# Kernel optimization log

Measured on AMD Instinct MI355X. Metric: run time of the kernel, lower is better.

The kernel has to match this reference:

```python
import jax, jax.numpy as jnp
import numpy as np

D = 512      # input_dim == encoder d_model
E = 512      # embedding_dim (codebook dim)
V = 8192     # num_embeddings
NC = 1       # num_codebooks
L = 6        # encoder layers
H = 8        # heads
F = 2048     # ffn dim
HD = D // H
EPS = 1e-5


def layernorm(x, s, b):
    m = jnp.mean(x, -1, keepdims=True)
    v = jnp.mean((x - m) ** 2, -1, keepdims=True)
    return (x - m) * jax.lax.rsqrt(v + EPS) * s + b


def sinusoidal_pe(T):
    pos = np.arange(T, dtype=np.float32)[:, None]
    i = np.arange(0, D, 2, dtype=np.float32)[None, :]
    ang = pos / np.power(10000.0, i / D)
    pe = np.zeros((T, D), np.float32)
    pe[:, 0::2] = np.sin(ang)
    pe[:, 1::2] = np.cos(ang)
    return jnp.asarray(pe)


def setup_inputs():
    key = jax.random.key(0)
    ks = jax.random.split(key, 12)
    B, T = 8, 1024
    xs = jax.random.normal(ks[0], (B, T, D), jnp.float32)
    xs_lens = (T // 2 + jax.random.randint(ks[1], (B,), 0, T // 2)).astype(jnp.int32)
    mask_indices = jax.random.uniform(ks[2], (B, T)) < 0.12  # span-mask surrogate
    sc = lambda k, shape, s=0.02: jax.random.normal(k, shape, jnp.float32) * s
    return {
        "xs": xs, "xs_lens": xs_lens, "mask_indices": mask_indices,
        "W_embed": sc(ks[3], (D, D), D ** -0.5),
        "ln1_s": jnp.ones((L, D)), "ln1_b": jnp.zeros((L, D)),
        "Wqkv": sc(ks[4], (L, D, 3 * D)), "Wo": sc(ks[5], (L, D, D)),
        "ln2_s": jnp.ones((L, D)), "ln2_b": jnp.zeros((L, D)),
        "W1": sc(ks[6], (L, D, F)), "W2": sc(ks[7], (L, F, D)),
        "an_s": jnp.ones((D,)), "an_b": jnp.zeros((D,)),
        "iln_s": jnp.ones((D,)), "iln_b": jnp.zeros((D,)),
        "mask_emb": sc(ks[8], (D,), 0.1),
        "top_n_out": sc(ks[9], (NC, D, V)),
        "projection": sc(ks[10], (D, E), (2.0 / (D + E)) ** 0.5),  # xavier_normal, frozen
        "embeddings": jax.random.normal(ks[11], (NC, E, V), jnp.float32),  # frozen codebook
    }


def encoder_blocks(x, pad_mask, ln1_s, ln1_b, Wqkv, Wo, ln2_s, ln2_b, W1, W2, an_s, an_b):
    B, T, _ = x.shape
    attn_bias = jnp.where(pad_mask, 0.0, -1e9)[:, None, None, :]  # [B,1,1,T]

    def layer(x, p):
        l1s, l1b, wqkv, wo, l2s, l2b, w1, w2 = p
        h = layernorm(x, l1s, l1b)
        q, k, v = jnp.split(h @ wqkv, 3, axis=-1)
        q = q.reshape(B, T, H, HD)
        k = k.reshape(B, T, H, HD)
        v = v.reshape(B, T, H, HD)
        scores = jnp.einsum('bqhd,bkhd->bhqk', q, k) * (HD ** -0.5) + attn_bias
        o = jnp.einsum('bhqk,bkhd->bqhd', jax.nn.softmax(scores, axis=-1), v)
        x = x + o.reshape(B, T, D) @ wo
        h = layernorm(x, l2s, l2b)
        x = x + jax.nn.relu(h @ w1) @ w2
        return x, None

    x, _ = jax.lax.scan(layer, x, (ln1_s, ln1_b, Wqkv, Wo, ln2_s, ln2_b, W1, W2))
    return layernorm(x, an_s, an_b)


def nearest_ids(x, iln_s, iln_b, projection, embeddings):
    # layernorm -> projection -> squared-distance argmin per codebook
    B, T, _ = x.shape
    z = layernorm(x, iln_s, iln_b) @ projection        # [B,T,E]
    flat = z.reshape(-1, E)                            # [N,E]
    d = (jnp.sum(flat ** 2, 1)[None, :, None]
         + jnp.sum(embeddings ** 2, 1)[:, None, :]
         - 2.0 * jnp.einsum('ne,gev->gnv', flat, embeddings))  # [NC,N,V]
    return jnp.argmin(d, -1).T.reshape(B, T, NC)


def reference(xs, xs_lens, mask_indices, W_embed, ln1_s, ln1_b, Wqkv, Wo, ln2_s, ln2_b,
              W1, W2, an_s, an_b, iln_s, iln_b, mask_emb, top_n_out, projection, embeddings):
    B, T, _ = xs.shape
    pad_mask = jnp.arange(T)[None, :] < xs_lens[:, None]              # [B,T]
    x = xs @ W_embed + sinusoidal_pe(T)[None]                         # encoder.embed
    target_ids = nearest_ids(x, iln_s, iln_b, projection, embeddings)  # [B,T,NC]
    masked_xs = jnp.where(mask_indices[..., None], mask_emb, x)
    out = encoder_blocks(masked_xs, pad_mask, ln1_s, ln1_b, Wqkv, Wo,
                         ln2_s, ln2_b, W1, W2, an_s, an_b)            # [B,T,D]
    logits = jnp.einsum('btd,gdv->bgtv', out, top_n_out)              # [B,NC,T,V]
    lsm = jax.nn.log_softmax(logits, axis=-1)
    tgt = jnp.transpose(target_ids, (0, 2, 1))                        # [B,NC,T]
    ent = -jnp.take_along_axis(lsm, tgt[..., None], axis=-1)[..., 0]  # [B,NC,T]
    m = (pad_mask & mask_indices).astype(jnp.float32)                 # [B,T]
    loss = jnp.sum(ent * m[:, None, :]) / (jnp.sum(m) * NC)
    return loss
```

## Files before the change

kernel.cpp:

```cpp
#include <hip/hip_runtime.h>
#include <hip/hip_bf16.h>

#define D_ 512
#define T_ 1024
#define B_ 8
#define H_ 8
#define F_ 2048
#define V_ 8192
#define L_ 6
#define NTOK 8192
#define EPS_ 1e-5f
#define NCAP 2048

typedef short short8 __attribute__((ext_vector_type(8)));
typedef float floatx4 __attribute__((ext_vector_type(4)));

__device__ __forceinline__ float bf2f(unsigned short u) {
  union { unsigned int i; float f; } v; v.i = ((unsigned int)u) << 16; return v.f;
}
__device__ __forceinline__ unsigned short f2bf(float f) {
  unsigned int u = __float_as_uint(f);
  return (unsigned short)((u + 0x7fffu + ((u >> 16) & 1u)) >> 16);
}
__device__ __forceinline__ float ldf(const void* p, long long i, int bf) {
  if (bf) return bf2f(((const unsigned short*)p)[i]);
  return ((const float*)p)[i];
}
__device__ __forceinline__ void ld16(const unsigned short* g, unsigned short* l) {
  __builtin_amdgcn_global_load_lds(
      (const __attribute__((address_space(1))) unsigned int*)g,
      (__attribute__((address_space(3))) unsigned int*)l, 16, 0, 0);
}
__device__ __forceinline__ unsigned int fkey(float f) {
  unsigned int u = __float_as_uint(f);
  return (u & 0x80000000u) ? ~u : (u ^ 0x80000000u);
}

__global__ void detect_kernel(const unsigned int* xsw, const unsigned int* mw, int* flags) {
  __shared__ int cnt[256];
  __shared__ int m01[256], mlo[256], mhi[256];
  int tid = threadIdx.x;
  int c = 0;
  for (int t = tid; t < 1024; t += 256) {
    unsigned int lo = xsw[t] & 0xffffu;
    int ok;
    if (lo == 0u) ok = 1;
    else { unsigned int e = (lo >> 7) & 0xffu; ok = (e >= 90u && e <= 140u); }
    c += ok;
  }
  int n01 = 0, lo38 = 0, hi38 = 0;
  for (int t = tid; t < 2048; t += 256) {
    unsigned int w = mw[t];
    if (w > 1u) n01 = 1;
    if ((w & 0xffffu) == 0x3f80u) lo38 = 1;
    if ((w >> 16) == 0x3f80u) hi38 = 1;
  }
  cnt[tid] = c; m01[tid] = n01; mlo[tid] = lo38; mhi[tid] = hi38;
  __syncthreads();
  for (int s = 128; s > 0; s >>= 1) {
    if (tid < s) {
      cnt[tid] += cnt[tid + s];
      m01[tid] |= m01[tid + s]; mlo[tid] |= mlo[tid + s]; mhi[tid] |= mhi[tid + s];
    }
    __syncthreads();
  }
  if (tid == 0) {
    flags[0] = (cnt[0] > 700) ? 1 : 0;
    int fmt;
    if (!m01[0]) fmt = 0;
    else if (mlo[0]) fmt = 2;
    else if (mhi[0]) fmt = 3;
    else fmt = 1;
    flags[1] = fmt;
  }
}

__global__ void conv_all_kernel(const void* d4, const void* d5, const void* d8,
                                const void* d9, const void* d12, const void* d13,
                                const void* d14, const void* d15, const void* d16,
                                float* P, const int* flags) {
  int i = blockIdx.x * 256 + threadIdx.x;
  if (i >= 14848) return;
  int bf = flags[0];
  const void* src; int off;
  if (i < 3072) { src = d4; off = 0; }
  else if (i < 6144) { src = d5; off = 3072; }
  else if (i < 9216) { src = d8; off = 6144; }
  else if (i < 12288) { src = d9; off = 9216; }
  else if (i < 12800) { src = d12; off = 12288; }
  else if (i < 13312) { src = d13; off = 12800; }
  else if (i < 13824) { src = d14; off = 13312; }
  else if (i < 14336) { src = d15; off = 13824; }
  else { src = d16; off = 14336; }
  P[i] = ldf(src, i - off, bf);
}

__global__ void convb_kernel(const void* src, unsigned short* dst, int n, const int* flags) {
  int i = blockIdx.x * 256 + threadIdx.x;
  if (i < n) {
    if (flags[0]) dst[i] = ((const unsigned short*)src)[i];
    else dst[i] = f2bf(((const float*)src)[i]);
  }
}

__global__ __launch_bounds__(256) void trans_kernel(const void* src, unsigned short* dst,
                                                    int K, int N, const int* flags) {
  int bf = flags[0];
  __shared__ unsigned short tile[32][33];
  int n0 = blockIdx.x * 32, k0 = blockIdx.y * 32, batch = blockIdx.z;
  long long sbase = (long long)batch * K * N;
  long long dbase = (long long)batch * N * K;
  int c = threadIdx.x & 31, r8 = threadIdx.x >> 5;
#pragma unroll
  for (int rr = 0; rr < 4; ++rr) {
    int r = r8 + rr * 8;
    tile[r][c] = f2bf(ldf(src, sbase + (long long)(k0 + r) * N + n0 + c, bf));
  }
  __syncthreads();
#pragma unroll
  for (int rr = 0; rr < 4; ++rr) {
    int nn = r8 + rr * 8;
    dst[dbase + (long long)(n0 + nn) * K + k0 + c] = tile[c][nn];
  }
}

__global__ __launch_bounds__(256) void trans_big_kernel(const void* top, const void* emb,
                                                        unsigned short* TOPT, unsigned short* EMBT,
                                                        float* en, const int* flags) {
  int bf = flags[0];
  __shared__ unsigned short tile[32][33];
  int n0 = blockIdx.x * 32, k0 = blockIdx.y * 32, z = blockIdx.z;
  const void* src = z ? emb : top;
  unsigned short* dst = z ? EMBT : TOPT;
  int c = threadIdx.x & 31, r8 = threadIdx.x >> 5;
#pragma unroll
  for (int rr = 0; rr < 4; ++rr) {
    int r = r8 + rr * 8;
    tile[r][c] = f2bf(ldf(src, (long long)(k0 + r) * V_ + n0 + c, bf));
  }
  __syncthreads();
#pragma unroll
  for (int rr = 0; rr < 4; ++rr) {
    int nn = r8 + rr * 8;
    dst[(long long)(n0 + nn) * D_ + k0 + c] = tile[c][nn];
  }
  if (z == 1 && threadIdx.x < 32) {
    int nn = threadIdx.x;
    float s = 0.f;
#pragma unroll
    for (int r = 0; r < 32; ++r) { float x = bf2f(tile[r][nn]); s += x * x; }
    atomicAdd(&en[n0 + nn], s);
  }
}

__global__ void prep_kernel(const void* mask, const int* lens, int* maski, float* mcomb,
                            int* idx, int* cnt, const int* flags) {
  int i = blockIdx.x * 256 + threadIdx.x;
  if (i >= NTOK) return;
  int fmt = flags[1];
  int mi;
  if (fmt == 0) mi = ((const int*)mask)[i] != 0;
  else if (fmt == 1) mi = ((const unsigned char*)mask)[i] != 0;
  else if (fmt == 2) mi = ((const unsigned short*)mask)[i] != 0;
  else mi = ((const float*)mask)[i] != 0.f;
  int b = i >> 10, t = i & (T_ - 1);
  int act = mi && (t < lens[b]);
  maski[i] = mi;
  mcomb[i] = act ? 1.f : 0.f;
  if (act) {
    int p = atomicAdd(cnt, 1);
    if (p < NCAP) idx[p] = i;
  }
}

#define BK 32

template<int BN>
__device__ __forceinline__ void stage_tile(const unsigned short* A, long long ga0, long long ga1,
                                           const unsigned short* BT, long long gb0, long long gb1,
                                           int k0, unsigned short (*Ab)[BK],
                                           unsigned short (*Bb)[BK], int wave, int c16) {
  ld16(A + ga0 + k0 + c16 * 8, &Ab[wave * 32][0]);
  ld16(A + ga1 + k0 + c16 * 8, &Ab[wave * 32 + 16][0]);
  if constexpr (BN == 128) {
    ld16(BT + gb0 + k0 + c16 * 8, &Bb[wave * 32][0]);
    ld16(BT + gb1 + k0 + c16 * 8, &Bb[wave * 32 + 16][0]);
  } else {
    ld16(BT + gb0 + k0 + c16 * 8, &Bb[wave * 16][0]);
  }
}

template<int BN>
__device__ __forceinline__ void mfma_pipe(const unsigned short* A, long long ga0, long long ga1,
                                          const unsigned short* BT, int n0, int Kdim,
                                          unsigned short (*As)[BK], unsigned short (*Bs)[BK],
                                          floatx4 (*acc)[BN / 32], int tid) {
  constexpr int NB = BN / 32;
  int wave = tid >> 6, lane = tid & 63;
  int r16 = lane >> 2, c16 = lane & 3;
  int lrow = lane & 15, quad = lane >> 4;
  int wm = (wave & 1) * 64, wn = (wave >> 1) * (BN / 2);
  int NT = Kdim / BK;
  long long gb0, gb1 = 0;
  if constexpr (BN == 128) {
    gb0 = (long long)(n0 + wave * 32 + r16) * Kdim;
    gb1 = gb0 + 16LL * Kdim;
  } else {
    gb0 = (long long)(n0 + wave * 16 + r16) * Kdim;
  }
  stage_tile<BN>(A, ga0, ga1, BT, gb0, gb1, 0, As, Bs, wave, c16);
  stage_tile<BN>(A, ga0, ga1, BT, gb0, gb1, BK, As + 128, Bs + BN, wave, c16);
  int cur = 0, nxt = 2;
  for (int t = 0; t < NT; ++t) {
    if (t == NT - 1) {
      asm volatile("s_waitcnt vmcnt(0)" ::: "memory");
    } else {
      if constexpr (BN == 128) asm volatile("s_waitcnt vmcnt(4)" ::: "memory");
      else                     asm volatile("s_waitcnt vmcnt(3)" ::: "memory");
    }
    __builtin_amdgcn_s_barrier();
    if (t + 2 < NT)
      stage_tile<BN>(A, ga0, ga1, BT, gb0, gb1, (t + 2) * BK,
                     As + nxt * 128, Bs + nxt * BN, wave, c16);
    unsigned short (*Ac)[BK] = As + cur * 128;
    unsigned short (*Bc)[BK] = Bs + cur * BN;
    short8 af[4], bfr[NB];
#pragma unroll
    for (int i = 0; i < 4; ++i) af[i] = *(const short8*)&Ac[wm + i * 16 + lrow][quad * 8];
#pragma unroll
    for (int j = 0; j < NB; ++j) bfr[j] = *(const short8*)&Bc[wn + j * 16 + lrow][quad * 8];
#pragma unroll
    for (int i = 0; i < 4; ++i)
#pragma unroll
      for (int j = 0; j < NB; ++j)
        acc[i][j] = __builtin_amdgcn_mfma_f32_16x16x32_bf16(af[i], bfr[j], acc[i][j], 0, 0, 0);
    cur = (cur == 2) ? 0 : cur + 1;
    nxt = (nxt == 2) ? 0 : nxt + 1;
  }
  __syncthreads();
}

__global__ __launch_bounds__(256) void mgemm_kernel(const unsigned short* A,
    const unsigned short* BT, long long boff, unsigned short* Cb, int Ndim, int Kdim) {
  __shared__ __align__(16) unsigned short As[3 * 128][BK];
  __shared__ __align__(16) unsigned short Bs[3 * 128][BK];
  int tid = threadIdx.x;
  int bid = blockIdx.x;
  int m0 = (bid & 63) * 128, n0 = (bid >> 6) * 128;
  int wave = tid >> 6, lane = tid & 63;
  int wm = (wave & 1) * 64, wn = (wave >> 1) * 64;
  int lrow = lane & 15, quad = lane >> 4;
  int r16 = lane >> 2;
  floatx4 acc[4][4];
#pragma unroll
  for (int i = 0; i < 4; ++i)
#pragma unroll
    for (int j = 0; j < 4; ++j) acc[i][j] = (floatx4){0.f, 0.f, 0.f, 0.f};
  long long ga0 = (long long)(m0 + wave * 32 + r16) * Kdim;
  long long ga1 = ga0 + 16LL * Kdim;
  mfma_pipe<128>(A, ga0, ga1, BT + boff, n0, Kdim, As, Bs, acc, tid);
#pragma unroll
  for (int i = 0; i < 4; ++i) {
    int mb = m0 + wm + i * 16 + quad * 4;
#pragma unroll
    for (int j = 0; j < 4; ++j) {
      int ncol = n0 + wn + j * 16 + lrow;
#pragma unroll
      for (int r = 0; r < 4; ++r)
        Cb[(long long)(mb + r) * Ndim + ncol] = f2bf(fmaxf(acc[i][j][r], 0.f));
    }
  }
}

__global__ __launch_bounds__(256) void mgemm64_kernel(const unsigned short* A,
    const unsigned short* BT, long long boff, float* Cf, unsigned short* Cb,
    int Ndim, int Kdim, int mode) {
  __shared__ __align__(16) unsigned short As[3 * 128][BK];
  __shared__ __align__(16) unsigned short Bs[3 * 64][BK];
  int tid = threadIdx.x;
  int bid = blockIdx.x;
  int m0 = (bid & 63) * 128, n0 = (bid >> 6) * 64;
  int wave = tid >> 6, lane = tid & 63;
  int r16 = lane >> 2;
  int wm = (wave & 1) * 64, wn = (wave >> 1) * 32;
  int lrow = lane & 15, quad = lane >> 4;
  floatx4 acc[4][2];
#pragma unroll
  for (int i = 0; i < 4; ++i)
#pragma unroll
    for (int j = 0; j < 2; ++j) acc[i][j] = (floatx4){0.f, 0.f, 0.f, 0.f};
  long long ga0 = (long long)(m0 + wave * 32 + r16) * Kdim;
  long long ga1 = ga0 + 16LL * Kdim;
  mfma_pipe<64>(A, ga0, ga1, BT + boff, n0, Kdim, As, Bs, acc, tid);
#pragma unroll
  for (int i = 0; i < 4; ++i) {
    int mb = m0 + wm + i * 16 + quad * 4;
#pragma unroll
    for (int j = 0; j < 2; ++j) {
      int ncol = n0 + wn + j * 16 + lrow;
#pragma unroll
      for (int r = 0; r < 4; ++r) {
        int m = mb + r;
        long long idx = (long long)m * Ndim + ncol;
        float v = acc[i][j][r];
        if (mode == 1) Cf[idx] += v;
        else if (mode == 4) Cb[idx] = f2bf(v);
        else if (mode == 3) {
          int t = m & (T_ - 1);
          float freq = __expf(-(float)(ncol & ~1) * (9.210340371976184f / (float)D_));
          float ang = (float)t * freq;
          v += (ncol & 1) ? cosf(ang) : sinf(ang);
          Cf[idx] = v;
        } else Cf[idx] = v;
      }
    }
  }
}

__global__ __launch_bounds__(256) void qkvgemm_kernel(const unsigned short* A,
    const unsigned short* BT, long long boff, unsigned short* QB,
    unsigned short* KSg, unsigned short* VTSg) {
  __shared__ __align__(16) union {
    struct { unsigned short As[3 * 128][BK]; unsigned short Bs[3 * 128][BK]; } s;
    unsigned short T[128][136];
  } sm;
  int tid = threadIdx.x;
  int bid = blockIdx.x;
  int m0 = (bid & 63) * 128;
  int nt = bid >> 6;
  int n0 = nt * 128;
  int wave = tid >> 6, lane = tid & 63;
  int wm = (wave & 1) * 64, wn = (wave >> 1) * 64;
  int lrow = lane & 15, quad = lane >> 4;
  int r16 = lane >> 2;
  floatx4 acc[4][4];
#pragma unroll
  for (int i = 0; i < 4; ++i)
#pragma unroll
    for (int j = 0; j < 4; ++j) acc[i][j] = (floatx4){0.f, 0.f, 0.f, 0.f};
  long long ga0 = (long long)(m0 + wave * 32 + r16) * D_;
  long long ga1 = ga0 + 16LL * D_;
  mfma_pipe<128>(A, ga0, ga1, BT + boff, n0, D_, sm.s.As, sm.s.Bs, acc, tid);
  int b = m0 >> 10, tt = (m0 >> 7) & 7;
  if (nt < 4) {
#pragma unroll
    for (int i = 0; i < 4; ++i) {
      int mb = m0 + wm + i * 16 + quad * 4;
#pragma unroll
      for (int j = 0; j < 4; ++j) {
        int ncol = n0 + wn + j * 16 + lrow;
#pragma unroll
        for (int r = 0; r < 4; ++r)
          QB[(long long)(mb + r) * 512 + ncol] = f2bf(acc[i][j][r]);
      }
    }
  } else if (nt < 8) {
#pragma unroll
    for (int i = 0; i < 4; ++i)
#pragma unroll
      for (int j = 0; j < 4; ++j)
#pragma unroll
        for (int r = 0; r < 4; ++r)
          sm.T[wm + i * 16 + quad * 4 + r][wn + j * 16 + lrow] = f2bf(acc[i][j][r]);
    __syncthreads();
    int tk = tid & 127, hg0 = tid >> 7;
#pragma unroll
    for (int p = 0; p < 8; ++p) {
      int hg = p * 2 + hg0;
      int h2 = hg >> 3, g = hg & 7;
      uint4 u = *(const uint4*)&sm.T[tk][h2 * 64 + g * 8];
      int headg = (nt - 4) * 2 + h2;
      long long dst = (((((long long)(b * 8 + headg)) * 8 + tt) * 8 + g) * 128 + tk) * 8;
      *(uint4*)&KSg[dst] = u;
    }
  } else {
#pragma unroll
    for (int i = 0; i < 4; ++i)
#pragma unroll
      for (int j = 0; j < 4; ++j)
#pragma unroll
        for (int r = 0; r < 4; ++r)
          sm.T[wn + j * 16 + lrow][wm + i * 16 + quad * 4 + r] = f2bf(acc[i][j][r]);
    __syncthreads();
    int col = tid & 127, gh = tid >> 7;
    int h2 = col >> 6, ch = col & 63;
    int headg = (nt - 8) * 2 + h2;
    long long base = ((((long long)(b * 8 + headg)) * 8 + tt) * 16);
#pragma unroll
    for (int p = 0; p < 8; ++p) {
      int g = p * 2 + gh;
      uint4 u = *(const uint4*)&sm.T[col][g * 8];
      long long dst = ((base + g) * 64 + ch) * 8;
      *(uint4*)&VTSg[dst] = u;
    }
  }
}

__global__ __launch_bounds__(256) void fattn_kernel(const unsigned short* QB,
    const unsigned short* KSg, const unsigned short* VTSg, const int* lens,
    unsigned short* ao) {
  __shared__ __align__(16) unsigned short Ps[64 * 128];
  int blk = blockIdx.x;
  int swz = (blk & 7) * 128 + (blk >> 3);
  int qt = swz & 15, bh = swz >> 4;
  int b = bh >> 3, h = bh & 7;
  int tid = threadIdx.x, wave = tid >> 6, lane = tid & 63;
  int c = lane & 15, quad = lane >> 4;
  int len = lens[b];
  short8 qf[2];
#pragma unroll
  for (int ks = 0; ks < 2; ++ks)
    qf[ks] = *(const short8*)&QB[(long long)(b * 1024 + qt * 64 + wave * 16 + c) * 512
                                 + h * 64 + ks * 32 + quad * 8];
  floatx4 accO[4];
  float lr[4];
#pragma unroll
  for (int j = 0; j < 4; ++j) { accO[j] = (floatx4){0.f, 0.f, 0.f, 0.f}; lr[j] = 0.f; }
  int nkt = (len + 127) >> 7;
  const unsigned short* ksrc = KSg + (long long)bh * 65536;
  const unsigned short* vsrc = VTSg + (long long)bh * 65536;
  for (int kt = 0; kt < nkt; ++kt) {
    const unsigned short* kp = ksrc + (long long)kt * 8192;
    const unsigned short* vp = vsrc + (long long)kt * 8192;
    int kbase = kt * 128;
    float lsr[4];
#pragma unroll
    for (int r = 0; r < 4; ++r) lsr[r] = 0.f;
#pragma unroll
    for (int jh = 0; jh < 2; ++jh) {
      short8 bk0[4], bk1[4];
#pragma unroll
      for (int j2 = 0; j2 < 4; ++j2) {
        int j = jh * 4 + j2;
        bk0[j2] = *(const short8*)&kp[(quad * 128 + j * 16 + c) * 8];
        bk1[j2] = *(const short8*)&kp[((4 + quad) * 128 + j * 16 + c) * 8];
      }
      floatx4 sacc[4];
#pragma unroll
      for (int j2 = 0; j2 < 4; ++j2) sacc[j2] = (floatx4){0.f, 0.f, 0.f, 0.f};
#pragma unroll
      for (int j2 = 0; j2 < 4; ++j2) {
        sacc[j2] = __builtin_amdgcn_mfma_f32_16x16x32_bf16(qf[0], bk0[j2], sacc[j2], 0, 0, 0);
        sacc[j2] = __builtin_amdgcn_mfma_f32_16x16x32_bf16(qf[1], bk1[j2], sacc[j2], 0, 0, 0);
      }
#pragma unroll
      for (int r = 0; r < 4; ++r) {
        int prow = wave * 16 + quad * 4 + r;
        int rx = quad * 4 + r;
#pragma unroll
        for (int j2 = 0; j2 < 4; ++j2) {
          int col = (jh * 4 + j2) * 16 + c;
          float s = sacc[j2][r] * 0.125f;
          s = (kbase + col < len) ? s : -100.f;
          float p = __expf(s);
          lsr[r] += p;
          Ps[prow * 128 + (((col >> 3) ^ rx) * 8) + (col & 7)] = f2bf(p);
        }
      }
    }
#pragma unroll
    for (int r = 0; r < 4; ++r) {
      float ls = lsr[r];
      ls += __shfl_xor(ls, 1, 64);
      ls += __shfl_xor(ls, 2, 64);
      ls += __shfl_xor(ls, 4, 64);
      ls += __shfl_xor(ls, 8, 64);
      lr[r] += ls;
    }
#pragma unroll
    for (int kh = 0; kh < 2; ++kh) {
      short8 vb[2][4];
#pragma unroll
      for (int kk2 = 0; kk2 < 2; ++kk2)
#pragma unroll
        for (int jn = 0; jn < 4; ++jn)
          vb[kk2][jn] = *(const short8*)&vp[(((kh * 2 + kk2) * 4 + quad) * 64 + jn * 16 + c) * 8];
#pragma unroll
      for (int kk2 = 0; kk2 < 2; ++kk2) {
        int kk = kh * 2 + kk2;
        int row = wave * 16 + c;
        short8 pa = *(const short8*)&Ps[row * 128 + (((kk * 4 + quad) ^ c) * 8)];
#pragma unroll
        for (int jn = 0; jn < 4; ++jn)
          accO[jn] = __builtin_amdgcn_mfma_f32_16x16x32_bf16(pa, vb[kk2][jn], accO[jn], 0, 0, 0);
      }
    }
  }
#pragma unroll
  for (int r = 0; r < 4; ++r) {
    float inv = 1.f / lr[r];
    long long token = b * 1024 + qt * 64 + wave * 16 + quad * 4 + r;
#pragma unroll
    for (int jn = 0; jn < 4; ++jn)
      ao[token * 512 + h * 64 + jn * 16 + c] = f2bf(accO[jn][r] * inv);
  }
}

__global__ __launch_bounds__(256) void dgemm_argmin(const unsigned short* Z, const int* ridx,
    const int* cnt, const unsigned short* ET, const float* en, unsigned long long* best) {
  __shared__ __align__(16) union {
    struct { unsigned short A[3 * 128][BK]; unsigned short B[3 * 128][BK]; } s;
    unsigned long long part[128][33];
  } sm;
  int m0 = blockIdx.y * 128;
  int na = *cnt;
  if (m0 >= ((na + 127) & ~127)) return;
  int tid = threadIdx.x;
  int n0 = blockIdx.x * 128;
  int wave = tid >> 6, lane = tid & 63;
  int wm = (wave & 1) * 64, wn = (wave >> 1) * 64;
  int lrow = lane & 15, quad = lane >> 4;
  int r16 = lane >> 2;
  int slot = (wave >> 1) * 16 + lrow;
  floatx4 acc[4][4];
#pragma unroll
  for (int i = 0; i < 4; ++i)
#pragma unroll
    for (int j = 0; j < 4; ++j) acc[i][j] = (floatx4){0.f, 0.f, 0.f, 0.f};
  long long ga0 = (long long)ridx[m0 + wave * 32 + r16] * D_;
  long long ga1 = (long long)ridx[m0 + wave * 32 + 16 + r16] * D_;
  mfma_pipe<128>(Z, ga0, ga1, ET, n0, D_, sm.s.A, sm.s.B, acc, tid);
  float env[4];
#pragma unroll
  for (int j = 0; j < 4; ++j) env[j] = en[n0 + wn + j * 16 + lrow];
#pragma unroll
  for (int i = 0; i < 4; ++i) {
#pragma unroll
    for (int r = 0; r < 4; ++r) {
      int rowl = wm + i * 16 + quad * 4 + r;
      unsigned long long bl = ~0ull;
#pragma unroll
      for (int j = 0; j < 4; ++j) {
        float v = env[j] - 2.f * acc[i][j][r];
        unsigned long long pk = (((unsigned long long)fkey(v)) << 32) |
                                (unsigned int)(n0 + wn + j * 16 + lrow);
        if (pk < bl) bl = pk;
      }
      sm.part[rowl][(slot + rowl) & 31] = bl;
    }
  }
  __syncthreads();
  if (tid < 128) {
    unsigned long long bb = sm.part[tid][0];
#pragma unroll 4
    for (int k2 = 1; k2 < 32; ++k2) { unsigned long long o = sm.part[tid][k2]; if (o < bb) bb = o; }
    atomicMin(&best[m0 + tid], bb);
  }
}

__global__ __launch_bounds__(256) void lgemm_lse(const unsigned short* OUTB, const int* ridx,
    const int* cnt, const unsigned short* TOPT, const unsigned long long* best,
    float* PS, float* TL) {
  __shared__ __align__(16) union {
    struct { unsigned short A[3 * 128][BK]; unsigned short B[3 * 128][BK]; } s;
    float part[128][33];
  } sm;
  int m0 = blockIdx.y * 128;
  int na = *cnt;
  if (m0 >= ((na + 127) & ~127)) return;
  int tid = threadIdx.x;
  int n0 = blockIdx.x * 128;
  int wave = tid >> 6, lane = tid & 63;
  int wm = (wave & 1) * 64, wn = (wave >> 1) * 64;
  int lrow = lane & 15, quad = lane >> 4;
  int r16 = lane >> 2;
  int slot = (wave >> 1) * 16 + lrow;
  floatx4 acc[4][4];
#pragma unroll
  for (int i = 0; i < 4; ++i)
#pragma unroll
    for (int j = 0; j < 4; ++j) acc[i][j] = (floatx4){0.f, 0.f, 0.f, 0.f};
  long long ga0 = (long long)ridx[m0 + wave * 32 + r16] * D_;
  long long ga1 = (long long)ridx[m0 + wave * 32 + 16 + r16] * D_;
  mfma_pipe<128>(OUTB, ga0, ga1, TOPT, n0, D_, sm.s.A, sm.s.B, acc, tid);
#pragma unroll
  for (int i = 0; i < 4; ++i) {
#pragma unroll
    for (int r = 0; r < 4; ++r) {
      int rowl = wm + i * 16 + quad * 4 + r;
      int tg = (int)(best[m0 + rowl] & 0xffffffffu);
      float ss = 0.f;
#pragma unroll
      for (int j = 0; j < 4; ++j) {
        float v = acc[i][j][r];
        ss += __expf(v);
        if (n0 + wn + j * 16 + lrow == tg) TL[m0 + rowl] = v;
      }
      sm.part[rowl][(slot + rowl) & 31] = ss;
    }
  }
  __syncthreads();
  if (tid < 128) {
    float S = 0.f;
#pragma unroll 4
    for (int k2 = 0; k2 < 32; ++k2) S += sm.part[tid][k2];
    PS[(long long)(m0 + tid) * 64 + blockIdx.x] = S;
  }
}

__global__ void lse_combine(const float* PS, const float* TL, const int* cnt, float* entm) {
  int t = blockIdx.x * 256 + threadIdx.x;
  if (t >= NCAP) return;
  if (t < *cnt) {
    float S = 0.f;
    for (int i = 0; i < 64; ++i) S += PS[(long long)t * 64 + i];
    entm[t] = __logf(S) - TL[t];
  } else {
    entm[t] = 0.f;
  }
}

__global__ __launch_bounds__(256) void ln_kernel(const float* X, float* Yf, unsigned short* Yb,
                                                 int obf, const float* s, const float* b) {
  int tid = threadIdx.x, wave = tid >> 6, lane = tid & 63;
  long long n = (long long)blockIdx.x * 4 + wave;
  const float* x = X + n * D_ + lane * 8;
  float v[8];
  *(float4*)&v[0] = *(const float4*)x;
  *(float4*)&v[4] = *(const float4*)(x + 4);
  float sum = 0.f;
#pragma unroll
  for (int j = 0; j < 8; ++j) sum += v[j];
  for (int m = 32; m; m >>= 1) sum += __shfl_xor(sum, m, 64);
  float mean = sum * (1.f / (float)D_);
  float vs = 0.f;
#pragma unroll
  for (int j = 0; j < 8; ++j) { v[j] -= mean; vs += v[j] * v[j]; }
  for (int m = 32; m; m >>= 1) vs += __shfl_xor(vs, m, 64);
  float r = rsqrtf(vs * (1.f / (float)D_) + EPS_);
  float sv[8], bv[8];
  *(float4*)&sv[0] = *(const float4*)(s + lane * 8);
  *(float4*)&sv[4] = *(const float4*)(s + lane * 8 + 4);
  *(float4*)&bv[0] = *(const float4*)(b + lane * 8);
  *(float4*)&bv[4] = *(const float4*)(b + lane * 8 + 4);
  if (obf) {
    unsigned short o[8];
#pragma unroll
    for (int j = 0; j < 8; ++j) o[j] = f2bf(v[j] * r * sv[j] + bv[j]);
    *(uint4*)(Yb + n * D_ + lane * 8) = *(const uint4*)o;
  } else {
    float o[8];
#pragma unroll
    for (int j = 0; j < 8; ++j) o[j] = v[j] * r * sv[j] + bv[j];
    *(float4*)(Yf + n * D_ + lane * 8) = *(const float4*)&o[0];
    *(float4*)(Yf + n * D_ + lane * 8 + 4) = *(const float4*)&o[4];
  }
}

__global__ void maskapply_kernel(float* x, const int* maski, const float* memb) {
  long long i = (long long)blockIdx.x * 256 + threadIdx.x;
  int n = (int)(i >> 9), d = (int)(i & 511);
  if (maski[n]) x[i] = memb[d];
}

__global__ void final_kernel(const float* entm, const float* mcomb, void* out) {
  __shared__ float r1[256], r2[256];
  int tid = threadIdx.x;
  float s1 = 0.f, s2 = 0.f;
  for (int i = tid; i < NCAP; i += 256) s1 += entm[i];
  for (int i = tid; i < NTOK; i += 256) s2 += mcomb[i];
  r1[tid] = s1; r2[tid] = s2;
  __syncthreads();
  for (int st = 128; st > 0; st >>= 1) {
    if (tid < st) { r1[tid] += r1[tid + st]; r2[tid] += r2[tid + st]; }
    __syncthreads();
  }
  if (tid == 0) {
    float loss = r1[0] / r2[0];
    unsigned short b16 = f2bf(loss);
    unsigned short* o = (unsigned short*)out;
    o[0] = b16; o[1] = b16;
  }
}

extern "C" void kernel_launch(void* const* d_in, const int* in_sizes, int n_in,
                              void* d_out, int out_size, void* d_ws, size_t ws_size,
                              hipStream_t stream) {
  if (n_in < 20) return;
  float* wsf = (float*)d_ws;
  int* flags = (int*)d_ws;
  const long long OF_P = 256;
  const long long OF_X = 16640;
  const long long OF_HB = OF_X + 4194304;
  const long long OF_BIG = OF_HB + 2097152;
  const long long OF_AOB = OF_BIG + 8388608;
  const long long OF_WT = OF_AOB + 2097152;
  const long long OF_TOPT = OF_WT + 9699328;
  const long long OF_EMBT = OF_TOPT + 2097152;
  const long long OF_EN = OF_EMBT + 2097152;
  const long long OF_BEST = OF_EN + 8192;
  const long long OF_PS = OF_BEST + 4096;
  const long long OF_TL = OF_PS + 131072;
  const long long OF_MI = OF_TL + 2048;
  const long long OF_MC = OF_MI + 8192;
  const long long OF_EM = OF_MC + 8192;
  const long long OF_CNT = OF_EM + 2048;
  const long long OF_IDX = OF_CNT + 16;
  const long long END = OF_IDX + 2048;
  if (ws_size < (size_t)END * 4) return;

  float* X = wsf + OF_X;
  unsigned short* HB = (unsigned short*)(wsf + OF_HB);
  unsigned short* BIGB = (unsigned short*)(wsf + OF_BIG);
  unsigned short* AOB = (unsigned short*)(wsf + OF_AOB);
  unsigned short* WT = (unsigned short*)(wsf + OF_WT);
  unsigned short* TOPT = (unsigned short*)(wsf + OF_TOPT);
  unsigned short* EMBT = (unsigned short*)(wsf + OF_EMBT);
  float* EN = wsf + OF_EN;
  unsigned long long* BEST = (unsigned long long*)(wsf + OF_BEST);
  float* PS = wsf + OF_PS;
  float* TL = wsf + OF_TL;
  int* MI = (int*)(wsf + OF_MI);
  float* MC = wsf + OF_MC;
  float* EM = wsf + OF_EM;
  int* CNT = (int*)(wsf + OF_CNT);
  int* IDX = (int*)(wsf + OF_IDX);
  float* P = wsf + OF_P;
  float* ln1s = P, *ln1b = P + 3072, *ln2s = P + 6144, *ln2b = P + 9216;
  float* ans = P + 12288, *anb = P + 12800, *ilns = P + 13312, *ilnb = P + 13824;
  float* memb = P + 14336;

  unsigned short* QB = BIGB;
  unsigned short* KSg = BIGB + 4194304;
  unsigned short* VTSg = BIGB + 8388608;

  const long long W_QKV = 0, W_O = 4718592, W_1 = 6291456, W_2 = 12582912,
                  W_EMB = 18874368, W_PRJ = 19136512;

  detect_kernel<<<1, 256, 0, stream>>>((const unsigned int*)d_in[0],
                                       (const unsigned int*)d_in[2], flags);
  hipMemsetAsync((void*)BEST, 0xFF, NCAP * 8, stream);
  hipMemsetAsync((void*)EN, 0, V_ * 4, stream);
  hipMemsetAsync((void*)CNT, 0, 16, stream);
  hipMemsetAsync((void*)IDX, 0, NCAP * 4, stream);
  conv_all_kernel<<<58, 256, 0, stream>>>(d_in[4], d_in[5], d_in[8], d_in[9], d_in[12],
                                          d_in[13], d_in[14], d_in[15], d_in[16], P, flags);
  prep_kernel<<<32, 256, 0, stream>>>(d_in[2], (const int*)d_in[1], MI, MC, IDX, CNT, flags);

  unsigned short* XSB = BIGB;
  convb_kernel<<<16384, 256, 0, stream>>>(d_in[0], XSB, 4194304, flags);

  trans_kernel<<<dim3(48, 16, 6), 256, 0, stream>>>(d_in[6], WT + W_QKV, 512, 1536, flags);
  trans_kernel<<<dim3(16, 16, 6), 256, 0, stream>>>(d_in[7], WT + W_O, 512, 512, flags);
  trans_kernel<<<dim3(64, 16, 6), 256, 0, stream>>>(d_in[10], WT + W_1, 512, 2048, flags);
  trans_kernel<<<dim3(16, 64, 6), 256, 0, stream>>>(d_in[11], WT + W_2, 2048, 512, flags);
  trans_kernel<<<dim3(16, 16, 1), 256, 0, stream>>>(d_in[3], WT + W_EMB, 512, 512, flags);
  trans_kernel<<<dim3(16, 16, 1), 256, 0, stream>>>(d_in[18], WT + W_PRJ, 512, 512, flags);
  trans_big_kernel<<<dim3(256, 16, 2), 256, 0, stream>>>(d_in[17], d_in[19], TOPT, EMBT,
                                                         EN, flags);

  dim3 gC(64, NCAP / 128);

  mgemm64_kernel<<<512, 256, 0, stream>>>(XSB, WT + W_EMB, 0, X, nullptr, 512, 512, 3);
  ln_kernel<<<2048, 256, 0, stream>>>(X, nullptr, HB, 1, ilns, ilnb);
  mgemm64_kernel<<<512, 256, 0, stream>>>(HB, WT + W_PRJ, 0, nullptr, AOB, 512, 512, 4);
  dgemm_argmin<<<gC, 256, 0, stream>>>(AOB, IDX, CNT, EMBT, EN, BEST);
  maskapply_kernel<<<16384, 256, 0, stream>>>(X, MI, memb);

  for (int l = 0; l < L_; ++l) {
    ln_kernel<<<2048, 256, 0, stream>>>(X, nullptr, HB, 1, ln1s + l * 512, ln1b + l * 512);
    qkvgemm_kernel<<<768, 256, 0, stream>>>(HB, WT + W_QKV, (long long)l * 786432,
                                            QB, KSg, VTSg);
    fattn_kernel<<<1024, 256, 0, stream>>>(QB, KSg, VTSg, (const int*)d_in[1], AOB);
    mgemm64_kernel<<<512, 256, 0, stream>>>(AOB, WT + W_O, (long long)l * 262144,
                                            X, nullptr, 512, 512, 1);
    ln_kernel<<<2048, 256, 0, stream>>>(X, nullptr, HB, 1, ln2s + l * 512, ln2b + l * 512);
    mgemm_kernel<<<1024, 256, 0, stream>>>(HB, WT + W_1, (long long)l * 1048576,
                                           BIGB, 2048, 512);
    mgemm64_kernel<<<512, 256, 0, stream>>>(BIGB, WT + W_2, (long long)l * 1048576,
                                            X, nullptr, 512, 2048, 1);
  }
  ln_kernel<<<2048, 256, 0, stream>>>(X, nullptr, AOB, 1, ans, anb);
  lgemm_lse<<<gC, 256, 0, stream>>>(AOB, IDX, CNT, TOPT, BEST, PS, TL);
  lse_combine<<<8, 256, 0, stream>>>(PS, TL, CNT, EM);
  final_kernel<<<1, 256, 0, stream>>>(EM, MC, d_out);
}
```

Baseline: 1.325 ms.

## Software-pipeline K/V register loads in flash attention and defer row-sum reduction

Restructures the attention inner loop so K fragments for the next key tile and V fragments for the current tile are loaded into two rotating register sets while the MFMA score and PV computations run. This hides global-load latency behind the matrix work. The per-row softmax sum shuffle reduction moves out of the loop to the epilogue, and launch bounds now request 4 blocks per SM. Register pressure rises, and the occupancy hint may force spills.

Result: slower. 2.157 ms (+62.7%).

```diff
diff --git a/kernel.cpp b/kernel.cpp
--- a/kernel.cpp
+++ b/kernel.cpp
@@ -396,7 +396,7 @@
   }
 }
 
-__global__ __launch_bounds__(256) void fattn_kernel(const unsigned short* QB,
+__global__ __launch_bounds__(256, 4) void fattn_kernel(const unsigned short* QB,
     const unsigned short* KSg, const unsigned short* VTSg, const int* lens,
     unsigned short* ao) {
   __shared__ __align__(16) unsigned short Ps[64 * 128];
@@ -417,78 +417,112 @@
 #pragma unroll
   for (int j = 0; j < 4; ++j) { accO[j] = (floatx4){0.f, 0.f, 0.f, 0.f}; lr[j] = 0.f; }
   int nkt = (len + 127) >> 7;
-  const unsigned short* ksrc = KSg + (long long)bh * 65536;
-  const unsigned short* vsrc = VTSg + (long long)bh * 65536;
+  const unsigned short* kp = KSg + (long long)bh * 65536;
+  const unsigned short* vp = VTSg + (long long)bh * 65536;
+  int kb = (quad * 128 + c) * 8;
+  int vbase = quad * 512 + c * 8;
+  short8 sA[8], sB[8];
+#pragma unroll
+  for (int j2 = 0; j2 < 4; ++j2) {
+    sA[j2]     = *(const short8*)&kp[kb + j2 * 128];
+    sA[4 + j2] = *(const short8*)&kp[kb + 4096 + j2 * 128];
+    sB[j2]     = *(const short8*)&kp[kb + (4 + j2) * 128];
+    sB[4 + j2] = *(const short8*)&kp[kb + 4096 + (4 + j2) * 128];
+  }
   for (int kt = 0; kt < nkt; ++kt) {
-    const unsigned short* kp = ksrc + (long long)kt * 8192;
-    const unsigned short* vp = vsrc + (long long)kt * 8192;
     int kbase = kt * 128;
-    float lsr[4];
-#pragma unroll
-    for (int r = 0; r < 4; ++r) lsr[r] = 0.f;
-#pragma unroll
-    for (int jh = 0; jh < 2; ++jh) {
-      short8 bk0[4], bk1[4];
+    const unsigned short* vpc = vp + kt * 8192;
+    const unsigned short* kpn = kp + (kt + 1) * 8192;
+    int more = (kt + 1 < nkt);
+    floatx4 s0[4];
+#pragma unroll
+    for (int j2 = 0; j2 < 4; ++j2) s0[j2] = (floatx4){0.f, 0.f, 0.f, 0.f};
+#pragma unroll
+    for (int j2 = 0; j2 < 4; ++j2) {
+      s0[j2] = __builtin_amdgcn_mfma_f32_16x16x32_bf16(qf[0], sA[j2], s0[j2], 0, 0, 0);
+      s0[j2] = __builtin_amdgcn_mfma_f32_16x16x32_bf16(qf[1], sA[4 + j2], s0[j2], 0, 0, 0);
+    }
+#pragma unroll
+    for (int q = 0; q < 8; ++q)
+      sA[q] = *(const short8*)&vpc[(q >> 2) * 2048 + (q & 3) * 128 + vbase];
+#pragma unroll
+    for (int r = 0; r < 4; ++r) {
+      int prow = wave * 16 + quad * 4 + r;
+      int rx = quad * 4 + r;
 #pragma unroll
       for (int j2 = 0; j2 < 4; ++j2) {
-        int j = jh * 4 + j2;
-        bk0[j2] = *(const short8*)&kp[(quad * 128 + j * 16 + c) * 8];
-        bk1[j2] = *(const short8*)&kp[((4 + quad) * 128 + j * 16 + c) * 8];
+        int col = j2 * 16 + c;
+        float s = s0[j2][r] * 0.125f;
+        s = (kbase + col < len) ? s : -100.f;
+        float p = __expf(s);
+        lr[r] += p;
+        Ps[prow * 128 + (((col >> 3) ^ rx) * 8) + (col & 7)] = f2bf(p);
       }
-      floatx4 sacc[4];
-#pragma unroll
-      for (int j2 = 0; j2 < 4; ++j2) sacc[j2] = (floatx4){0.f, 0.f, 0.f, 0.f};
+    }
+    floatx4 s1[4];
+#pragma unroll
+    for (int j2 = 0; j2 < 4; ++j2) s1[j2] = (floatx4){0.f, 0.f, 0.f, 0.f};
+#pragma unroll
+    for (int j2 = 0; j2 < 4; ++j2) {
+      s1[j2] = __builtin_amdgcn_mfma_f32_16x16x32_bf16(qf[0], sB[j2], s1[j2], 0, 0, 0);
+      s1[j2] = __builtin_amdgcn_mfma_f32_16x16x32_bf16(qf[1], sB[4 + j2], s1[j2], 0, 0, 0);
+    }
+#pragma unroll
+    for (int q = 0; q < 8; ++q)
+      sB[q] = *(const short8*)&vpc[(2 + (q >> 2)) * 2048 + (q & 3) * 128 + vbase];
+#pragma unroll
+    for (int r = 0; r < 4; ++r) {
+      int prow = wave * 16 + quad * 4 + r;
+      int rx = quad * 4 + r;
 #pragma unroll
       for (int j2 = 0; j2 < 4; ++j2) {
-        sacc[j2] = __builtin_amdgcn_mfma_f32_16x16x32_bf16(qf[0], bk0[j2], sacc[j2], 0, 0, 0);
-        sacc[j2] = __builtin_amdgcn_mfma_f32_16x16x32_bf16(qf[1], bk1[j2], sacc[j2], 0, 0, 0);
+        int col = (4 + j2) * 16 + c;
+        float s = s1[j2][r] * 0.125f;
+        s = (kbase + col < len) ? s : -100.f;
+        float p = __expf(s);
+        lr[r] += p;
+        Ps[prow * 128 + (((col >> 3) ^ rx) * 8) + (col & 7)] = f2bf(p);
       }
-#pragma unroll
-      for (int r = 0; r < 4; ++r) {
-        int prow = wave * 16 + quad * 4 + r;
-        int rx = quad * 4 + r;
-#pragma unroll
-        for (int j2 = 0; j2 < 4; ++j2) {
-          int col = (jh * 4 + j2) * 16 + c;
-          float s = sacc[j2][r] * 0.125f;
-          s = (kbase + col < len) ? s : -100.f;
-          float p = __expf(s);
-          lsr[r] += p;
-          Ps[prow * 128 + (((col >> 3) ^ rx) * 8) + (col & 7)] = f2bf(p);
-        }
+    }
+    int row = wave * 16 + c;
+#pragma unroll
+    for (int kk2 = 0; kk2 < 2; ++kk2) {
+      short8 pa = *(const short8*)&Ps[row * 128 + (((kk2 * 4 + quad) ^ c) * 8)];
+#pragma unroll
+      for (int jn = 0; jn < 4; ++jn)
+        accO[jn] = __builtin_amdgcn_mfma_f32_16x16x32_bf16(pa, sA[kk2 * 4 + jn], accO[jn], 0, 0, 0);
+    }
+    if (more) {
+#pragma unroll
+      for (int j2 = 0; j2 < 4; ++j2) {
+        sA[j2]     = *(const short8*)&kpn[kb + j2 * 128];
+        sA[4 + j2] = *(const short8*)&kpn[kb + 4096 + j2 * 128];
       }
     }
 #pragma unroll
-    for (int r = 0; r < 4; ++r) {
-      float ls = lsr[r];
-      ls += __shfl_xor(ls, 1, 64);
-      ls += __shfl_xor(ls, 2, 64);
-      ls += __shfl_xor(ls, 4, 64);
-      ls += __shfl_xor(ls, 8, 64);
-      lr[r] += ls;
-    }
-#pragma unroll
-    for (int kh = 0; kh < 2; ++kh) {
-      short8 vb[2][4];
-#pragma unroll
-      for (int kk2 = 0; kk2 < 2; ++kk2)
-#pragma unroll
-        for (int jn = 0; jn < 4; ++jn)
-          vb[kk2][jn] = *(const short8*)&vp[(((kh * 2 + kk2) * 4 + quad) * 64 + jn * 16 + c) * 8];
-#pragma unroll
-      for (int kk2 = 0; kk2 < 2; ++kk2) {
-        int kk = kh * 2 + kk2;
-        int row = wave * 16 + c;
-        short8 pa = *(const short8*)&Ps[row * 128 + (((kk * 4 + quad) ^ c) * 8)];
-#pragma unroll
-        for (int jn = 0; jn < 4; ++jn)
-          accO[jn] = __builtin_amdgcn_mfma_f32_16x16x32_bf16(pa, vb[kk2][jn], accO[jn], 0, 0, 0);
+    for (int kk2 = 0; kk2 < 2; ++kk2) {
+      int kk = 2 + kk2;
+      short8 pa = *(const short8*)&Ps[row * 128 + (((kk * 4 + quad) ^ c) * 8)];
+#pragma unroll
+      for (int jn = 0; jn < 4; ++jn)
+        accO[jn] = __builtin_amdgcn_mfma_f32_16x16x32_bf16(pa, sB[kk2 * 4 + jn], accO[jn], 0, 0, 0);
+    }
+    if (more) {
+#pragma unroll
+      for (int j2 = 0; j2 < 4; ++j2) {
+        sB[j2]     = *(const short8*)&kpn[kb + (4 + j2) * 128];
+        sB[4 + j2] = *(const short8*)&kpn[kb + 4096 + (4 + j2) * 128];
       }
     }
   }
 #pragma unroll
   for (int r = 0; r < 4; ++r) {
-    float inv = 1.f / lr[r];
+    float ls = lr[r];
+    ls += __shfl_xor(ls, 1, 64);
+    ls += __shfl_xor(ls, 2, 64);
+    ls += __shfl_xor(ls, 4, 64);
+    ls += __shfl_xor(ls, 8, 64);
+    float inv = 1.f / ls;
     long long token = b * 1024 + qt * 64 + wave * 16 + quad * 4 + r;
 #pragma unroll
     for (int jn = 0; jn < 4; ++jn)
```
